# Optimization experiments

Measured on AMD Instinct MI355X. Metric: run time of the kernel, lower is better.

The kernel has to match this reference:

```python
import jax, jax.numpy as jnp
import numpy as np

B, Q, C, V = 512, 100, 81, 117  # batch, queries, obj classes (80+no-object), verbs
THRES, ALPHA, BETA = 0.7, 1.0, 0.5


def setup_inputs() -> dict:
    key = jax.random.key(0)
    k1, k2, k3, k4, k5, k6 = jax.random.split(key, 6)
    out_obj_logits = jax.random.normal(k1, (B, Q, C), jnp.float32)
    out_verb_logits = jax.random.normal(k2, (B, Q, V), jnp.float32)
    out_sub_boxes = jax.random.uniform(k3, (B, Q, 4), jnp.float32)
    out_obj_boxes = jax.random.uniform(k4, (B, Q, 4), jnp.float32)
    # correct_mat: binary verb-object compatibility [V, C-1] + ones column for no-object slot -> [V, C]
    cm = (jax.random.uniform(k5, (V, C - 1)) < 0.3).astype(jnp.float32)
    correct_mat = jnp.concatenate([cm, jnp.ones((V, 1), jnp.float32)], axis=1)
    target_sizes = jax.random.randint(k6, (B, 2), 480, 1334).astype(jnp.int64)
    return {
        'out_obj_logits': out_obj_logits,
        'out_verb_logits': out_verb_logits,
        'out_sub_boxes': out_sub_boxes,
        'out_obj_boxes': out_obj_boxes,
        'correct_mat': correct_mat,
        'target_sizes': target_sizes,
    }


def _box_cxcywh_to_xyxy(b):
    cx, cy, w, h = b[..., 0], b[..., 1], b[..., 2], b[..., 3]
    return jnp.stack([cx - 0.5 * w, cy - 0.5 * h, cx + 0.5 * w, cy + 0.5 * h], axis=-1)


def _pairwise_iou(boxes):  # boxes [Q,4] xyxy (pixel coords, +1 convention as in source)
    x1, y1, x2, y2 = boxes[:, 0], boxes[:, 1], boxes[:, 2], boxes[:, 3]
    area = (x2 - x1 + 1.0) * (y2 - y1 + 1.0)
    xx1 = jnp.maximum(x1[:, None], x1[None, :])
    yy1 = jnp.maximum(y1[:, None], y1[None, :])
    xx2 = jnp.minimum(x2[:, None], x2[None, :])
    yy2 = jnp.minimum(y2[:, None], y2[None, :])
    w = jnp.maximum(0.0, xx2 - xx1 + 1.0)
    h = jnp.maximum(0.0, yy2 - yy1 + 1.0)
    inter = w * h
    union = area[:, None] + area[None, :] - inter
    return inter / union


def _nms_one_image(sub_b, obj_b, obj_lab, max_scores):
    # Greedy pairwise triplet NMS. Grouping key in the source degenerates to the
    # object label alone (subject cat is constant, verb-label string identical),
    # so suppression applies only between detections with the same object label.
    order = jnp.argsort(-max_scores)
    sb, ob, lab = sub_b[order], obj_b[order], obj_lab[order]
    ovr = jnp.power(_pairwise_iou(sb), ALPHA) * jnp.power(_pairwise_iou(ob), BETA)
    upper = jnp.triu(jnp.ones((Q, Q), bool), 1)
    sup_mat = upper & (lab[:, None] == lab[None, :]) & (ovr > THRES)

    def body(i, supp):
        return supp | (sup_mat[i] & jnp.logical_not(supp[i]))

    supp = jax.lax.fori_loop(0, Q, body, jnp.zeros((Q,), bool))
    keep = jnp.zeros((Q,), bool).at[order].set(jnp.logical_not(supp))
    return keep  # in original query order


def reference(out_obj_logits, out_verb_logits, out_sub_boxes, out_obj_boxes, correct_mat, target_sizes):
    obj_prob = jax.nn.softmax(out_obj_logits, axis=-1)
    obj_scores = obj_prob[..., :-1].max(axis=-1)            # [B,Q]
    obj_labels = obj_prob[..., :-1].argmax(axis=-1)         # [B,Q]
    verb_scores = jax.nn.sigmoid(out_verb_logits)           # [B,Q,V]

    ts = target_sizes.astype(jnp.float32)
    img_h, img_w = ts[:, 0], ts[:, 1]
    scale_fct = jnp.stack([img_w, img_h, img_w, img_h], axis=1)  # [B,4]
    sub_boxes = _box_cxcywh_to_xyxy(out_sub_boxes) * scale_fct[:, None, :]
    obj_boxes = _box_cxcywh_to_xyxy(out_obj_boxes) * scale_fct[:, None, :]

    # masks[b,q,v] = correct_mat[v, obj_labels[b,q]]
    masks = correct_mat.T[obj_labels]                        # [B,Q,V]
    hoi_scores = verb_scores * obj_scores[..., None] * masks

    max_scores = hoi_scores.max(axis=-1)                     # [B,Q]
    keep = jax.vmap(_nms_one_image)(sub_boxes, obj_boxes, obj_labels, max_scores)
    return hoi_scores, obj_labels, sub_boxes, obj_boxes, keep
```

## Files before the change

kernel.cpp:

```cpp
#include <hip/hip_runtime.h>
#include <math.h>

#define Bn 512
#define Qn 100
#define Cn 81
#define Vn 117
#define NQ (Bn * Qn)

#define OFF_HOI  0
#define OFF_LAB  (NQ * Vn)
#define OFF_SUB  (OFF_LAB + NQ)
#define OFF_OBJ  (OFF_SUB + NQ * 4)
#define OFF_KEEP (OFF_OBJ + NQ * 4)

__global__ __launch_bounds__(256) void hoi_k1(
    const float* __restrict__ obj_logits,
    const float* __restrict__ verb_logits,
    const float* __restrict__ sub_boxes,
    const float* __restrict__ obj_boxes,
    const float* __restrict__ correct_mat,
    const int*   __restrict__ target_sizes,
    float* __restrict__ out)
{
    const int wave = threadIdx.x >> 6;
    const int lane = threadIdx.x & 63;
    const int idx  = blockIdx.x * 4 + wave;
    const int b    = idx / Qn;

    const float NEG = -3.4e38f;

    const float* lg = obj_logits + (size_t)idx * Cn;
    float l0 = (lane < Cn)      ? lg[lane]      : NEG;
    float l1 = (lane + 64 < Cn) ? lg[lane + 64] : NEG;

    float m = fmaxf(l0, l1);
    #pragma unroll
    for (int o = 32; o; o >>= 1) m = fmaxf(m, __shfl_xor(m, o, 64));

    float s = (lane < Cn      ? expf(l0 - m) : 0.f)
            + (lane + 64 < Cn ? expf(l1 - m) : 0.f);
    #pragma unroll
    for (int o = 32; o; o >>= 1) s += __shfl_xor(s, o, 64);

    float v   = (lane < Cn - 1) ? l0 : NEG;
    int   vid = lane;
    if ((lane + 64 < Cn - 1) && l1 > v) { v = l1; vid = lane + 64; }
    #pragma unroll
    for (int o = 32; o; o >>= 1) {
        float ov = __shfl_xor(v, o, 64);
        int   oi = __shfl_xor(vid, o, 64);
        if (ov > v || (ov == v && oi < vid)) { v = ov; vid = oi; }
    }
    const int   label     = vid;
    const float obj_score = expf(v - m) / s;

    const float* vlg = verb_logits + (size_t)idx * Vn;
    float* hoi = out + OFF_HOI + (size_t)idx * Vn;
    float mx = 0.f;
    #pragma unroll
    for (int rep = 0; rep < 2; rep++) {
        int j = lane + rep * 64;
        if (j < Vn) {
            float x  = vlg[j];
            float sg = 1.f / (1.f + expf(-x));
            float h  = sg * obj_score * correct_mat[j * Cn + label];
            hoi[j] = h;
            mx = fmaxf(mx, h);
        }
    }
    #pragma unroll
    for (int o = 32; o; o >>= 1) mx = fmaxf(mx, __shfl_xor(mx, o, 64));

    if (lane == 0) {
        out[OFF_LAB + idx]  = (float)label;
        out[OFF_KEEP + idx] = mx;
    }

    if (lane < 2) {
        float ih = (float)target_sizes[2 * b + 0];
        float iw = (float)target_sizes[2 * b + 1];
        const float4 bx = ((const float4*)(lane == 0 ? sub_boxes : obj_boxes))[idx];
        float4 r;
        r.x = (bx.x - 0.5f * bx.z) * iw;
        r.y = (bx.y - 0.5f * bx.w) * ih;
        r.z = (bx.x + 0.5f * bx.z) * iw;
        r.w = (bx.y + 0.5f * bx.w) * ih;
        ((float4*)(out + (lane == 0 ? OFF_SUB : OFF_OBJ)))[idx] = r;
    }
}

__global__ __launch_bounds__(128) void hoi_nms(float* __restrict__ out)
{
    __shared__ float score[Qn];
    __shared__ int   order[Qn];
    __shared__ float sx1[Qn], sy1[Qn], sx2[Qn], sy2[Qn], sarea[Qn];
    __shared__ float ox1[Qn], oy1[Qn], ox2[Qn], oy2[Qn], oarea[Qn];
    __shared__ int   lab[Qn];
    __shared__ int   supp[Qn];

    const int b = blockIdx.x;
    const int t = threadIdx.x;

    if (t < Qn) score[t] = out[OFF_KEEP + b * Qn + t];
    __syncthreads();

    if (t < Qn) {
        float si = score[t];
        int rank = 0;
        for (int j = 0; j < Qn; j++) {
            float sj = score[j];
            rank += (sj > si) || (sj == si && j < t);
        }
        order[rank] = t;
    }
    __syncthreads();

    if (t < Qn) {
        int o = order[t];
        float4 sb = ((const float4*)(out + OFF_SUB))[b * Qn + o];
        float4 ob = ((const float4*)(out + OFF_OBJ))[b * Qn + o];
        sx1[t] = sb.x; sy1[t] = sb.y; sx2[t] = sb.z; sy2[t] = sb.w;
        sarea[t] = (sb.z - sb.x + 1.f) * (sb.w - sb.y + 1.f);
        ox1[t] = ob.x; oy1[t] = ob.y; ox2[t] = ob.z; oy2[t] = ob.w;
        oarea[t] = (ob.z - ob.x + 1.f) * (ob.w - ob.y + 1.f);
        lab[t]  = (int)out[OFF_LAB + b * Qn + o];
        supp[t] = 0;
    }
    __syncthreads();

    for (int i = 0; i < Qn - 1; i++) {
        if (!supp[i] && t > i && t < Qn && lab[t] == lab[i]) {
            float w = fmaxf(0.f, fminf(sx2[i], sx2[t]) - fmaxf(sx1[i], sx1[t]) + 1.f);
            float h = fmaxf(0.f, fminf(sy2[i], sy2[t]) - fmaxf(sy1[i], sy1[t]) + 1.f);
            float inter = w * h;
            float iou_s = inter / (sarea[i] + sarea[t] - inter);
            w = fmaxf(0.f, fminf(ox2[i], ox2[t]) - fmaxf(ox1[i], ox1[t]) + 1.f);
            h = fmaxf(0.f, fminf(oy2[i], oy2[t]) - fmaxf(oy1[i], oy1[t]) + 1.f);
            inter = w * h;
            float iou_o = inter / (oarea[i] + oarea[t] - inter);
            if (iou_s * sqrtf(iou_o) > 0.7f) supp[t] = 1;
        }
        __syncthreads();
    }

    if (t < Qn) out[OFF_KEEP + b * Qn + order[t]] = supp[t] ? 0.f : 1.f;
}

extern "C" void kernel_launch(void* const* d_in, const int* in_sizes, int n_in,
                              void* d_out, int out_size, void* d_ws, size_t ws_size,
                              hipStream_t stream) {
    const float* obj_logits   = (const float*)d_in[0];
    const float* verb_logits  = (const float*)d_in[1];
    const float* sub_boxes    = (const float*)d_in[2];
    const float* obj_boxes    = (const float*)d_in[3];
    const float* correct_mat  = (const float*)d_in[4];
    const int*   target_sizes = (const int*)d_in[5];
    float* out = (float*)d_out;

    hoi_k1<<<NQ / 4, 256, 0, stream>>>(obj_logits, verb_logits, sub_boxes,
                                       obj_boxes, correct_mat, target_sizes, out);
    hoi_nms<<<Bn, 128, 0, stream>>>(out);
}
```

Measured before the change: 148.7 us.

## Make NMS wave-per-image without barriers, use fast math and transposed correct_mat

The NMS kernel now assigns one wavefront per image, with four images per block. It keeps suppression flags in registers and broadcasts them with shuffles, which removes the per-iteration block barrier, and it packs boxes, areas and labels into float4 shared arrays. The first kernel drops the max subtraction in the softmax and uses fast exp and hardware reciprocal. It also reads a correct_mat transposed once into workspace, so the per-row reads are contiguous. Skipping the max subtraction risks overflow for large logits, and the fast reciprocal and exp may change results slightly near the threshold.

```diff
diff --git a/kernel.cpp b/kernel.cpp
--- a/kernel.cpp
+++ b/kernel.cpp
@@ -13,12 +13,21 @@
 #define OFF_OBJ  (OFF_SUB + NQ * 4)
 #define OFF_KEEP (OFF_OBJ + NQ * 4)
 
+__device__ __forceinline__ float frcp(float x) { return __builtin_amdgcn_rcpf(x); }
+
+__global__ __launch_bounds__(128) void cm_transpose(const float* __restrict__ cm,
+                                                    float* __restrict__ cmT) {
+    int c = blockIdx.x;
+    int v = threadIdx.x;
+    if (v < Vn) cmT[c * Vn + v] = cm[v * Cn + c];
+}
+
 __global__ __launch_bounds__(256) void hoi_k1(
     const float* __restrict__ obj_logits,
     const float* __restrict__ verb_logits,
     const float* __restrict__ sub_boxes,
     const float* __restrict__ obj_boxes,
-    const float* __restrict__ correct_mat,
+    const float* __restrict__ cmT,
     const int*   __restrict__ target_sizes,
     float* __restrict__ out)
 {
@@ -27,46 +36,43 @@
     const int idx  = blockIdx.x * 4 + wave;
     const int b    = idx / Qn;
 
-    const float NEG = -3.4e38f;
-
     const float* lg = obj_logits + (size_t)idx * Cn;
-    float l0 = (lane < Cn)      ? lg[lane]      : NEG;
-    float l1 = (lane + 64 < Cn) ? lg[lane + 64] : NEG;
-
-    float m = fmaxf(l0, l1);
-    #pragma unroll
-    for (int o = 32; o; o >>= 1) m = fmaxf(m, __shfl_xor(m, o, 64));
-
-    float s = (lane < Cn      ? expf(l0 - m) : 0.f)
-            + (lane + 64 < Cn ? expf(l1 - m) : 0.f);
-    #pragma unroll
-    for (int o = 32; o; o >>= 1) s += __shfl_xor(s, o, 64);
-
-    float v   = (lane < Cn - 1) ? l0 : NEG;
+    float l0 = lg[lane];
+    float l1 = (lane < Cn - 64) ? lg[lane + 64] : 0.f;
+
+    float v   = l0;
     int   vid = lane;
-    if ((lane + 64 < Cn - 1) && l1 > v) { v = l1; vid = lane + 64; }
+    if (lane < Cn - 1 - 64 && l1 > v) { v = l1; vid = lane + 64; }
     #pragma unroll
     for (int o = 32; o; o >>= 1) {
         float ov = __shfl_xor(v, o, 64);
         int   oi = __shfl_xor(vid, o, 64);
         if (ov > v || (ov == v && oi < vid)) { v = ov; vid = oi; }
     }
+
+    float e = __expf(l0) + ((lane < Cn - 64) ? __expf(l1) : 0.f);
+    #pragma unroll
+    for (int o = 32; o; o >>= 1) e += __shfl_xor(e, o, 64);
+
     const int   label     = vid;
-    const float obj_score = expf(v - m) / s;
-
-    const float* vlg = verb_logits + (size_t)idx * Vn;
+    const float obj_score = __expf(v) * frcp(e);
+
+    const float* crow = cmT + (size_t)label * Vn;
+    const float* vlg  = verb_logits + (size_t)idx * Vn;
     float* hoi = out + OFF_HOI + (size_t)idx * Vn;
+
     float mx = 0.f;
-    #pragma unroll
-    for (int rep = 0; rep < 2; rep++) {
-        int j = lane + rep * 64;
-        if (j < Vn) {
-            float x  = vlg[j];
-            float sg = 1.f / (1.f + expf(-x));
-            float h  = sg * obj_score * correct_mat[j * Cn + label];
-            hoi[j] = h;
-            mx = fmaxf(mx, h);
-        }
+    {
+        float x  = vlg[lane];
+        float h  = frcp(1.f + __expf(-x)) * obj_score * crow[lane];
+        hoi[lane] = h;
+        mx = fmaxf(mx, h);
+    }
+    if (lane + 64 < Vn) {
+        float x  = vlg[lane + 64];
+        float h  = frcp(1.f + __expf(-x)) * obj_score * crow[lane + 64];
+        hoi[lane + 64] = h;
+        mx = fmaxf(mx, h);
     }
     #pragma unroll
     for (int o = 32; o; o >>= 1) mx = fmaxf(mx, __shfl_xor(mx, o, 64));
@@ -89,61 +95,93 @@
     }
 }
 
-__global__ __launch_bounds__(128) void hoi_nms(float* __restrict__ out)
+__global__ __launch_bounds__(256) void hoi_nms(float* __restrict__ out)
 {
-    __shared__ float score[Qn];
-    __shared__ int   order[Qn];
-    __shared__ float sx1[Qn], sy1[Qn], sx2[Qn], sy2[Qn], sarea[Qn];
-    __shared__ float ox1[Qn], oy1[Qn], ox2[Qn], oy2[Qn], oarea[Qn];
-    __shared__ int   lab[Qn];
-    __shared__ int   supp[Qn];
-
-    const int b = blockIdx.x;
-    const int t = threadIdx.x;
-
-    if (t < Qn) score[t] = out[OFF_KEEP + b * Qn + t];
+    __shared__ float  sc[4][128];
+    __shared__ float4 SB[4][Qn];
+    __shared__ float4 OB[4][Qn];
+    __shared__ float4 MT[4][Qn];
+
+    const int w = threadIdx.x >> 6;
+    const int l = threadIdx.x & 63;
+    const int b = blockIdx.x * 4 + w;
+    const int t0 = l, t1 = 64 + l;
+    const bool v1 = (t1 < Qn);
+
+    const float* keep_in = out + OFF_KEEP + (size_t)b * Qn;
+    float s0 = keep_in[t0];
+    float s1 = v1 ? keep_in[t1] : 0.f;
+    sc[w][l]      = s0;
+    sc[w][64 + l] = v1 ? s1 : -1e38f;
     __syncthreads();
 
-    if (t < Qn) {
-        float si = score[t];
-        int rank = 0;
-        for (int j = 0; j < Qn; j++) {
-            float sj = score[j];
-            rank += (sj > si) || (sj == si && j < t);
+    int r0 = 0, r1 = 0;
+    for (int j = 0; j < Qn; j++) {
+        float sj = sc[w][j];
+        r0 += (sj > s0) || (sj == s0 && j < t0);
+        r1 += (sj > s1) || (sj == s1 && j < t1);
+    }
+
+    const float4* subp = (const float4*)(out + OFF_SUB) + (size_t)b * Qn;
+    const float4* objp = (const float4*)(out + OFF_OBJ) + (size_t)b * Qn;
+    const float*  labp = out + OFF_LAB + (size_t)b * Qn;
+    {
+        float4 sb = subp[t0], ob = objp[t0];
+        float4 mt;
+        mt.x = (sb.z - sb.x + 1.f) * (sb.w - sb.y + 1.f);
+        mt.y = (ob.z - ob.x + 1.f) * (ob.w - ob.y + 1.f);
+        mt.z = labp[t0];
+        mt.w = (float)t0;
+        SB[w][r0] = sb; OB[w][r0] = ob; MT[w][r0] = mt;
+    }
+    if (v1) {
+        float4 sb = subp[t1], ob = objp[t1];
+        float4 mt;
+        mt.x = (sb.z - sb.x + 1.f) * (sb.w - sb.y + 1.f);
+        mt.y = (ob.z - ob.x + 1.f) * (ob.w - ob.y + 1.f);
+        mt.z = labp[t1];
+        mt.w = (float)t1;
+        SB[w][r1] = sb; OB[w][r1] = ob; MT[w][r1] = mt;
+    }
+    __syncthreads();
+
+    float4 A0s = SB[w][t0], A0o = OB[w][t0], A0m = MT[w][t0];
+    float4 A1s, A1o, A1m;
+    if (v1) { A1s = SB[w][t1]; A1o = OB[w][t1]; A1m = MT[w][t1]; }
+
+    int sup0 = 0, sup1 = 0;
+    for (int i = 0; i < Qn - 1; i++) {
+        int mybit = (i < 64) ? sup0 : sup1;
+        int bit   = __shfl(mybit, i & 63, 64);
+        if (bit) continue;
+        float4 Bs = SB[w][i], Bo = OB[w][i], Bm = MT[w][i];
+        if (!sup0 && t0 > i && A0m.z == Bm.z) {
+            float ww = fmaxf(0.f, fminf(Bs.z, A0s.z) - fmaxf(Bs.x, A0s.x) + 1.f);
+            float hh = fmaxf(0.f, fminf(Bs.w, A0s.w) - fmaxf(Bs.y, A0s.y) + 1.f);
+            float inter = ww * hh;
+            float iou_s = inter / (Bm.x + A0m.x - inter);
+            ww = fmaxf(0.f, fminf(Bo.z, A0o.z) - fmaxf(Bo.x, A0o.x) + 1.f);
+            hh = fmaxf(0.f, fminf(Bo.w, A0o.w) - fmaxf(Bo.y, A0o.y) + 1.f);
+            inter = ww * hh;
+            float iou_o = inter / (Bm.y + A0m.y - inter);
+            if (iou_s * sqrtf(iou_o) > 0.7f) sup0 = 1;
         }
-        order[rank] = t;
-    }
-    __syncthreads();
-
-    if (t < Qn) {
-        int o = order[t];
-        float4 sb = ((const float4*)(out + OFF_SUB))[b * Qn + o];
-        float4 ob = ((const float4*)(out + OFF_OBJ))[b * Qn + o];
-        sx1[t] = sb.x; sy1[t] = sb.y; sx2[t] = sb.z; sy2[t] = sb.w;
-        sarea[t] = (sb.z - sb.x + 1.f) * (sb.w - sb.y + 1.f);
-        ox1[t] = ob.x; oy1[t] = ob.y; ox2[t] = ob.z; oy2[t] = ob.w;
-        oarea[t] = (ob.z - ob.x + 1.f) * (ob.w - ob.y + 1.f);
-        lab[t]  = (int)out[OFF_LAB + b * Qn + o];
-        supp[t] = 0;
-    }
-    __syncthreads();
-
-    for (int i = 0; i < Qn - 1; i++) {
-        if (!supp[i] && t > i && t < Qn && lab[t] == lab[i]) {
-            float w = fmaxf(0.f, fminf(sx2[i], sx2[t]) - fmaxf(sx1[i], sx1[t]) + 1.f);
-            float h = fmaxf(0.f, fminf(sy2[i], sy2[t]) - fmaxf(sy1[i], sy1[t]) + 1.f);
-            float inter = w * h;
-            float iou_s = inter / (sarea[i] + sarea[t] - inter);
-            w = fmaxf(0.f, fminf(ox2[i], ox2[t]) - fmaxf(ox1[i], ox1[t]) + 1.f);
-            h = fmaxf(0.f, fminf(oy2[i], oy2[t]) - fmaxf(oy1[i], oy1[t]) + 1.f);
-            inter = w * h;
-            float iou_o = inter / (oarea[i] + oarea[t] - inter);
-            if (iou_s * sqrtf(iou_o) > 0.7f) supp[t] = 1;
+        if (v1 && !sup1 && t1 > i && A1m.z == Bm.z) {
+            float ww = fmaxf(0.f, fminf(Bs.z, A1s.z) - fmaxf(Bs.x, A1s.x) + 1.f);
+            float hh = fmaxf(0.f, fminf(Bs.w, A1s.w) - fmaxf(Bs.y, A1s.y) + 1.f);
+            float inter = ww * hh;
+            float iou_s = inter / (Bm.x + A1m.x - inter);
+            ww = fmaxf(0.f, fminf(Bo.z, A1o.z) - fmaxf(Bo.x, A1o.x) + 1.f);
+            hh = fmaxf(0.f, fminf(Bo.w, A1o.w) - fmaxf(Bo.y, A1o.y) + 1.f);
+            inter = ww * hh;
+            float iou_o = inter / (Bm.y + A1m.y - inter);
+            if (iou_s * sqrtf(iou_o) > 0.7f) sup1 = 1;
         }
-        __syncthreads();
-    }
-
-    if (t < Qn) out[OFF_KEEP + b * Qn + order[t]] = supp[t] ? 0.f : 1.f;
+    }
+
+    float* keep_out = out + OFF_KEEP + (size_t)b * Qn;
+    keep_out[(int)A0m.w] = sup0 ? 0.f : 1.f;
+    if (v1) keep_out[(int)A1m.w] = sup1 ? 0.f : 1.f;
 }
 
 extern "C" void kernel_launch(void* const* d_in, const int* in_sizes, int n_in,
@@ -156,8 +194,10 @@
     const float* correct_mat  = (const float*)d_in[4];
     const int*   target_sizes = (const int*)d_in[5];
     float* out = (float*)d_out;
-
+    float* cmT = (float*)d_ws;
+
+    cm_transpose<<<Cn, 128, 0, stream>>>(correct_mat, cmT);
     hoi_k1<<<NQ / 4, 256, 0, stream>>>(obj_logits, verb_logits, sub_boxes,
-                                       obj_boxes, correct_mat, target_sizes, out);
-    hoi_nms<<<Bn, 128, 0, stream>>>(out);
-}
+                                       obj_boxes, cmT, target_sizes, out);
+    hoi_nms<<<Bn / 4, 256, 0, stream>>>(out);
+}
```

Result: faster. 144.6 us (-2.8%).

## Rework HOI kernel mapping and replace serial NMS with bitmask suppression

Applied to the files above, without the earlier changes.

The first kernel now maps 16 lanes to each query instead of a full wave, uses fast exp and reciprocal intrinsics, drops the max-subtraction in the softmax, and reads a transposed correct_mat produced by a new small kernel. The NMS kernel computes the full pairwise suppression matrix in parallel with ballots into 64-bit row masks, then resolves greedy suppression with a per-thread bitmask scan instead of 99 barrier-separated steps. This targets underutilized lanes, uncoalesced correct_mat gathers and barrier-bound NMS. In exchange it adds an extra launch, and skipping the softmax max-shift can overflow or lose precision for large logits.

```diff
diff --git a/kernel.cpp b/kernel.cpp
--- a/kernel.cpp
+++ b/kernel.cpp
@@ -13,137 +13,163 @@
 #define OFF_OBJ  (OFF_SUB + NQ * 4)
 #define OFF_KEEP (OFF_OBJ + NQ * 4)
 
+__device__ __forceinline__ float frcp(float x) { return __builtin_amdgcn_rcpf(x); }
+
+__global__ __launch_bounds__(128) void cm_transpose(const float* __restrict__ cm,
+                                                    float* __restrict__ cmT) {
+    int c = blockIdx.x;
+    int v = threadIdx.x;
+    if (v < Vn) cmT[c * Vn + v] = cm[v * Cn + c];
+}
+
 __global__ __launch_bounds__(256) void hoi_k1(
     const float* __restrict__ obj_logits,
     const float* __restrict__ verb_logits,
     const float* __restrict__ sub_boxes,
     const float* __restrict__ obj_boxes,
-    const float* __restrict__ correct_mat,
+    const float* __restrict__ cmT,
     const int*   __restrict__ target_sizes,
     float* __restrict__ out)
 {
-    const int wave = threadIdx.x >> 6;
-    const int lane = threadIdx.x & 63;
-    const int idx  = blockIdx.x * 4 + wave;
-    const int b    = idx / Qn;
-
-    const float NEG = -3.4e38f;
+    const int t   = threadIdx.x & 15;
+    const int g   = threadIdx.x >> 4;
+    const int idx = blockIdx.x * 16 + g;
+    const int b   = idx / Qn;
 
     const float* lg = obj_logits + (size_t)idx * Cn;
-    float l0 = (lane < Cn)      ? lg[lane]      : NEG;
-    float l1 = (lane + 64 < Cn) ? lg[lane + 64] : NEG;
+    float l0 = lg[t], l1 = lg[t + 16], l2 = lg[t + 32], l3 = lg[t + 48], l4 = lg[t + 64];
+    float l5 = lg[80];
 
-    float m = fmaxf(l0, l1);
+    float v = l0; int vid = t;
+    if (l1 > v) { v = l1; vid = t + 16; }
+    if (l2 > v) { v = l2; vid = t + 32; }
+    if (l3 > v) { v = l3; vid = t + 48; }
+    if (l4 > v) { v = l4; vid = t + 64; }
     #pragma unroll
-    for (int o = 32; o; o >>= 1) m = fmaxf(m, __shfl_xor(m, o, 64));
-
-    float s = (lane < Cn      ? expf(l0 - m) : 0.f)
-            + (lane + 64 < Cn ? expf(l1 - m) : 0.f);
-    #pragma unroll
-    for (int o = 32; o; o >>= 1) s += __shfl_xor(s, o, 64);
-
-    float v   = (lane < Cn - 1) ? l0 : NEG;
-    int   vid = lane;
-    if ((lane + 64 < Cn - 1) && l1 > v) { v = l1; vid = lane + 64; }
-    #pragma unroll
-    for (int o = 32; o; o >>= 1) {
+    for (int o = 8; o; o >>= 1) {
         float ov = __shfl_xor(v, o, 64);
         int   oi = __shfl_xor(vid, o, 64);
         if (ov > v || (ov == v && oi < vid)) { v = ov; vid = oi; }
     }
+
+    float e = __expf(l0) + __expf(l1) + __expf(l2) + __expf(l3) + __expf(l4);
+    #pragma unroll
+    for (int o = 8; o; o >>= 1) e += __shfl_xor(e, o, 64);
+    e += __expf(l5);
+
     const int   label     = vid;
-    const float obj_score = expf(v - m) / s;
+    const float obj_score = __expf(v) * frcp(e);
 
-    const float* vlg = verb_logits + (size_t)idx * Vn;
+    const float* crow = cmT + (size_t)label * Vn;
+    const float* vlg  = verb_logits + (size_t)idx * Vn;
     float* hoi = out + OFF_HOI + (size_t)idx * Vn;
+
     float mx = 0.f;
     #pragma unroll
-    for (int rep = 0; rep < 2; rep++) {
-        int j = lane + rep * 64;
-        if (j < Vn) {
-            float x  = vlg[j];
-            float sg = 1.f / (1.f + expf(-x));
-            float h  = sg * obj_score * correct_mat[j * Cn + label];
-            hoi[j] = h;
+    for (int c = 0; c < 8; c++) {
+        int col = t + 16 * c;
+        if (col < Vn) {
+            float x = vlg[col];
+            float h = frcp(1.f + __expf(-x)) * obj_score * crow[col];
+            hoi[col] = h;
             mx = fmaxf(mx, h);
         }
     }
     #pragma unroll
-    for (int o = 32; o; o >>= 1) mx = fmaxf(mx, __shfl_xor(mx, o, 64));
+    for (int o = 8; o; o >>= 1) mx = fmaxf(mx, __shfl_xor(mx, o, 64));
 
-    if (lane == 0) {
+    if (t == 0) {
         out[OFF_LAB + idx]  = (float)label;
         out[OFF_KEEP + idx] = mx;
     }
 
-    if (lane < 2) {
+    if (t < 2) {
         float ih = (float)target_sizes[2 * b + 0];
         float iw = (float)target_sizes[2 * b + 1];
-        const float4 bx = ((const float4*)(lane == 0 ? sub_boxes : obj_boxes))[idx];
+        const float4 bx = ((const float4*)(t == 0 ? sub_boxes : obj_boxes))[idx];
         float4 r;
         r.x = (bx.x - 0.5f * bx.z) * iw;
         r.y = (bx.y - 0.5f * bx.w) * ih;
         r.z = (bx.x + 0.5f * bx.z) * iw;
         r.w = (bx.y + 0.5f * bx.w) * ih;
-        ((float4*)(out + (lane == 0 ? OFF_SUB : OFF_OBJ)))[idx] = r;
+        ((float4*)(out + (t == 0 ? OFF_SUB : OFF_OBJ)))[idx] = r;
     }
 }
 
 __global__ __launch_bounds__(128) void hoi_nms(float* __restrict__ out)
 {
-    __shared__ float score[Qn];
-    __shared__ int   order[Qn];
-    __shared__ float sx1[Qn], sy1[Qn], sx2[Qn], sy2[Qn], sarea[Qn];
-    __shared__ float ox1[Qn], oy1[Qn], ox2[Qn], oy2[Qn], oarea[Qn];
-    __shared__ int   lab[Qn];
-    __shared__ int   supp[Qn];
+    __shared__ float  sc[Qn];
+    __shared__ float4 SB[Qn], OB[Qn];
+    __shared__ float  AS[Qn], AO[Qn];
+    __shared__ int    LB[128];
+    __shared__ int    OI[Qn];
+    __shared__ unsigned long long ROW[Qn][2];
 
     const int b = blockIdx.x;
     const int t = threadIdx.x;
+    const int w = t >> 6;
 
-    if (t < Qn) score[t] = out[OFF_KEEP + b * Qn + t];
+    float* keepp = out + OFF_KEEP + (size_t)b * Qn;
+
+    if (t < Qn) { sc[t] = keepp[t]; ROW[t][0] = 0ull; ROW[t][1] = 0ull; }
+    if (t >= Qn) LB[t] = -1;
     __syncthreads();
 
     if (t < Qn) {
-        float si = score[t];
-        int rank = 0;
+        float s = sc[t];
+        int r = 0;
         for (int j = 0; j < Qn; j++) {
-            float sj = score[j];
-            rank += (sj > si) || (sj == si && j < t);
+            float sj = sc[j];
+            r += (sj > s) || (sj == s && j < t);
         }
-        order[rank] = t;
+        float4 sb = ((const float4*)(out + OFF_SUB))[b * Qn + t];
+        float4 ob = ((const float4*)(out + OFF_OBJ))[b * Qn + t];
+        SB[r] = sb; OB[r] = ob;
+        AS[r] = (sb.z - sb.x + 1.f) * (sb.w - sb.y + 1.f);
+        AO[r] = (ob.z - ob.x + 1.f) * (ob.w - ob.y + 1.f);
+        LB[r] = (int)out[OFF_LAB + b * Qn + t];
+        OI[r] = t;
     }
     __syncthreads();
 
-    if (t < Qn) {
-        int o = order[t];
-        float4 sb = ((const float4*)(out + OFF_SUB))[b * Qn + o];
-        float4 ob = ((const float4*)(out + OFF_OBJ))[b * Qn + o];
-        sx1[t] = sb.x; sy1[t] = sb.y; sx2[t] = sb.z; sy2[t] = sb.w;
-        sarea[t] = (sb.z - sb.x + 1.f) * (sb.w - sb.y + 1.f);
-        ox1[t] = ob.x; oy1[t] = ob.y; ox2[t] = ob.z; oy2[t] = ob.w;
-        oarea[t] = (ob.z - ob.x + 1.f) * (ob.w - ob.y + 1.f);
-        lab[t]  = (int)out[OFF_LAB + b * Qn + o];
-        supp[t] = 0;
+    const int  j  = t;
+    const bool jv = (j < Qn);
+    float4 js, jo; float jas = 0.f, jao = 0.f; int jlb = -2;
+    js = make_float4(0.f, 0.f, 0.f, 0.f); jo = js;
+    if (jv) { js = SB[j]; jo = OB[j]; jas = AS[j]; jao = AO[j]; jlb = LB[j]; }
+
+    const int iend = (w == 0) ? 63 : 99;
+    for (int i = 0; i < iend; i++) {
+        float4 is = SB[i], io = OB[i];
+        float  ias = AS[i], iao = AO[i];
+        int    ilb = LB[i];
+        float ww = fmaxf(0.f, fminf(is.z, js.z) - fmaxf(is.x, js.x) + 1.f);
+        float hh = fmaxf(0.f, fminf(is.w, js.w) - fmaxf(is.y, js.y) + 1.f);
+        float inter = ww * hh;
+        float iou_s = inter / (ias + jas - inter);
+        ww = fmaxf(0.f, fminf(io.z, jo.z) - fmaxf(io.x, jo.x) + 1.f);
+        hh = fmaxf(0.f, fminf(io.w, jo.w) - fmaxf(io.y, jo.y) + 1.f);
+        inter = ww * hh;
+        float iou_o = inter / (iao + jao - inter);
+        bool cond = jv && (j > i) && (jlb == ilb) && (iou_s * sqrtf(iou_o) > 0.7f);
+        unsigned long long m = __ballot(cond);
+        if ((t & 63) == 0) ROW[i][w] = m;
     }
     __syncthreads();
 
+    unsigned long long s0 = 0ull, s1 = 0ull;
+    #pragma unroll
     for (int i = 0; i < Qn - 1; i++) {
-        if (!supp[i] && t > i && t < Qn && lab[t] == lab[i]) {
-            float w = fmaxf(0.f, fminf(sx2[i], sx2[t]) - fmaxf(sx1[i], sx1[t]) + 1.f);
-            float h = fmaxf(0.f, fminf(sy2[i], sy2[t]) - fmaxf(sy1[i], sy1[t]) + 1.f);
-            float inter = w * h;
-            float iou_s = inter / (sarea[i] + sarea[t] - inter);
-            w = fmaxf(0.f, fminf(ox2[i], ox2[t]) - fmaxf(ox1[i], ox1[t]) + 1.f);
-            h = fmaxf(0.f, fminf(oy2[i], oy2[t]) - fmaxf(oy1[i], oy1[t]) + 1.f);
-            inter = w * h;
-            float iou_o = inter / (oarea[i] + oarea[t] - inter);
-            if (iou_s * sqrtf(iou_o) > 0.7f) supp[t] = 1;
-        }
-        __syncthreads();
+        unsigned long long dead = ((i < 64 ? s0 : s1) >> (i & 63)) & 1ull;
+        unsigned long long msk  = dead - 1ull;
+        s0 |= ROW[i][0] & msk;
+        s1 |= ROW[i][1] & msk;
     }
 
-    if (t < Qn) out[OFF_KEEP + b * Qn + order[t]] = supp[t] ? 0.f : 1.f;
+    if (t < Qn) {
+        unsigned long long bit = (t < 64 ? (s0 >> t) : (s1 >> (t - 64))) & 1ull;
+        keepp[OI[t]] = bit ? 0.f : 1.f;
+    }
 }
 
 extern "C" void kernel_launch(void* const* d_in, const int* in_sizes, int n_in,
@@ -156,8 +182,10 @@
     const float* correct_mat  = (const float*)d_in[4];
     const int*   target_sizes = (const int*)d_in[5];
     float* out = (float*)d_out;
+    float* cmT = (float*)d_ws;
 
-    hoi_k1<<<NQ / 4, 256, 0, stream>>>(obj_logits, verb_logits, sub_boxes,
-                                       obj_boxes, correct_mat, target_sizes, out);
+    cm_transpose<<<Cn, 128, 0, stream>>>(correct_mat, cmT);
+    hoi_k1<<<NQ / 16, 256, 0, stream>>>(obj_logits, verb_logits, sub_boxes,
+                                        obj_boxes, cmT, target_sizes, out);
     hoi_nms<<<Bn, 128, 0, stream>>>(out);
 }
```

Result: faster. 139.1 us (-6.5%).
